# Performance work log

Hardware: AMD Instinct MI355X
Metric: run time of the kernel (lower is better)

## Reference

```python
import jax, jax.numpy as jnp
import numpy as np

SR = 16000; HOP = 160; NM = 80; FMIN = 80.0; FMAX = 8000.0
T = 4 * SR              # 64000 samples
NSTAGE = 4              # cascaded biquad stages per channel
D = 256; NH = 8; DH = 32; NL = 8; DFF = 1024
BN_EPS = 1e-5; LN_EPS = 1e-5


def _biquad_coeffs():
    fc = np.logspace(np.log10(FMIN), np.log10(FMAX), NM)           # [NM]
    q = 4.0 + 2.0 * np.arange(NSTAGE)                               # [4]
    omega = 2.0 * np.pi * fc / SR
    alpha = np.sin(omega)[None, :] / (2.0 * q[:, None])             # [4,NM]
    a0 = 1.0 + alpha
    b0 = alpha / a0
    b2 = -alpha / a0
    a1 = (-2.0 * np.cos(omega))[None, :] / a0
    a2 = (1.0 - alpha) / a0
    return tuple(jnp.asarray(c, jnp.float32) for c in (b0, b2, a1, a2))


def _cochlear(x):
    # x: [B,T] -> [B,NM,T]; 4-stage cascaded bandpass biquads, zero initial state.
    b0, b2, a1, a2 = _biquad_coeffs()
    B = x.shape[0]
    z = jnp.zeros((NSTAGE, NM, B), x.dtype)

    def body(carry, xt):
        x1, x2, y1, y2 = carry                      # each [4,NM,B]
        sig = jnp.broadcast_to(xt[None, :], (NM, B))
        nx1, nx2, ny1, ny2 = [], [], [], []
        for s in range(NSTAGE):                     # fixed small cascade
            y = (b0[s][:, None] * sig + b2[s][:, None] * x2[s]
                 - a1[s][:, None] * y1[s] - a2[s][:, None] * y2[s])
            nx1.append(sig); nx2.append(x1[s]); ny1.append(y); ny2.append(y1[s])
            sig = y
        return (jnp.stack(nx1), jnp.stack(nx2), jnp.stack(ny1), jnp.stack(ny2)), sig

    _, ys = jax.lax.scan(body, (z, z, z, z), x.T)   # ys: [T,NM,B]
    return ys.transpose(2, 1, 0)


def _ln(x, g, b):
    m = x.mean(-1, keepdims=True)
    v = jnp.mean((x - m) ** 2, -1, keepdims=True)
    return (x - m) * jax.lax.rsqrt(v + LN_EPS) * g + b


def _cbr(h, w, b, g, bb):
    h = jax.lax.conv_general_dilated(h, w, (1, 1), 'SAME',
                                     dimension_numbers=('NCHW', 'OIHW', 'NCHW'))
    h = h + b[None, :, None, None]
    # eval-mode BatchNorm2d: running_mean=0, running_var=1
    h = h * (g / np.sqrt(1.0 + BN_EPS))[None, :, None, None] + bb[None, :, None, None]
    return jax.nn.relu(h)


def _mha(x, wqkv, bqkv, wo, bo):
    B, S, _ = x.shape
    qkv = x @ wqkv.T + bqkv
    q, k, v = jnp.split(qkv, 3, axis=-1)
    heads = lambda t: t.reshape(B, S, NH, DH).transpose(0, 2, 1, 3)
    q, k, v = heads(q), heads(k), heads(v)
    attn = jax.nn.softmax(jnp.einsum('bhqd,bhkd->bhqk', q, k) / np.sqrt(DH), axis=-1)
    o = jnp.einsum('bhqk,bhkd->bhqd', attn, v).transpose(0, 2, 1, 3).reshape(B, S, D)
    return o @ wo.T + bo


def _forward(x, cw1, cb1, g1, be1, cw2, cb2, g2, be2, cw3, cb3, g3, be3,
             qkv_w, qkv_b, out_w, out_b, ln1_g, ln1_b,
             ff1_w, ff1_b, ff2_w, ff2_b, ln2_g, ln2_b, pw, pb):
    B = x.shape[0]
    sig = _cochlear(x)                                    # [B,80,T]
    env = jnp.abs(sig)
    frames = env.reshape(B, NM, T // HOP, HOP).mean(-1)   # avg_pool1d k=s=160 -> [B,80,400]
    feats = jnp.log(frames + 1e-8)[:, None]               # [B,1,80,400]
    h = _cbr(feats, cw1, cb1, g1, be1)
    h = _cbr(h, cw2, cb2, g2, be2)
    h = _cbr(h, cw3, cb3, g3, be3)                        # [B,256,80,400]
    # AdaptiveAvgPool2d((80,32)): H already 80 (identity); pool W 400->32 with torch bin rule
    W_in, W_out = h.shape[-1], 32
    bins = [(int(np.floor(i * W_in / W_out)), int(np.ceil((i + 1) * W_in / W_out)))
            for i in range(W_out)]
    h = jnp.stack([h[..., s:e].mean(-1) for s, e in bins], axis=-1)   # [B,256,80,32]
    tok = h.reshape(B, D, -1).transpose(0, 2, 1)          # [B,2560,256]
    for l in range(NL):   # post-norm encoder layer, relu FFN, dropout=0 (eval)
        a = _mha(tok, qkv_w[l], qkv_b[l], out_w[l], out_b[l])
        tok = _ln(tok + a, ln1_g[l], ln1_b[l])
        f = jax.nn.relu(tok @ ff1_w[l].T + ff1_b[l]) @ ff2_w[l].T + ff2_b[l]
        tok = _ln(tok + f, ln2_g[l], ln2_b[l])
    return tok @ pw.T + pb                                # [B,2560,512]


def setup_inputs() -> dict:
    key = jax.random.key(0)
    ks = jax.random.split(key, 16)
    w = lambda k, shape, std=0.02: jax.random.normal(k, shape, jnp.float32) * std
    return {
        'x': jax.random.normal(ks[0], (1, T), jnp.float32),
        'cw1': w(ks[1], (64, 1, 3, 3), 0.1), 'cb1': jnp.zeros((64,)),
        'g1': jnp.ones((64,)), 'be1': jnp.zeros((64,)),
        'cw2': w(ks[2], (128, 64, 3, 3), 0.05), 'cb2': jnp.zeros((128,)),
        'g2': jnp.ones((128,)), 'be2': jnp.zeros((128,)),
        'cw3': w(ks[3], (256, 128, 3, 3), 0.05), 'cb3': jnp.zeros((256,)),
        'g3': jnp.ones((256,)), 'be3': jnp.zeros((256,)),
        'qkv_w': w(ks[4], (NL, 3 * D, D)), 'qkv_b': jnp.zeros((NL, 3 * D)),
        'out_w': w(ks[5], (NL, D, D)), 'out_b': jnp.zeros((NL, D)),
        'ln1_g': jnp.ones((NL, D)), 'ln1_b': jnp.zeros((NL, D)),
        'ff1_w': w(ks[6], (NL, DFF, D)), 'ff1_b': jnp.zeros((NL, DFF)),
        'ff2_w': w(ks[7], (NL, D, DFF)), 'ff2_b': jnp.zeros((NL, D)),
        'ln2_g': jnp.ones((NL, D)), 'ln2_b': jnp.zeros((NL, D)),
        'pw': w(ks[8], (512, D)), 'pb': jnp.zeros((512,)),
    }


def reference(x, cw1, cb1, g1, be1, cw2, cb2, g2, be2, cw3, cb3, g3, be3,
              qkv_w, qkv_b, out_w, out_b, ln1_g, ln1_b,
              ff1_w, ff1_b, ff2_w, ff2_b, ln2_g, ln2_b, pw, pb):
    return _forward(x, cw1, cb1, g1, be1, cw2, cb2, g2, be2, cw3, cb3, g3, be3,
                    qkv_w, qkv_b, out_w, out_b, ln1_g, ln1_b,
                    ff1_w, ff1_b, ff2_w, ff2_b, ln2_g, ln2_b, pw, pb)
```

## Files before the change

kernel.cpp:

```cpp
#include <hip/hip_runtime.h>
#include <hip/hip_bf16.h>
#include <math.h>

typedef __hip_bfloat16 bf16;
typedef short s16x8 __attribute__((ext_vector_type(8)));
typedef float f32x4 __attribute__((ext_vector_type(4)));

__device__ __forceinline__ float b2f(const bf16 v) { return __bfloat162float(v); }
__device__ __forceinline__ float ldf(int isbf, const void* p, size_t i) {
    return isbf ? __bfloat162float(((const bf16*)p)[i]) : ((const float*)p)[i];
}
__device__ __forceinline__ double ldd(int isbf, const void* p, size_t i) {
    return (double)ldf(isbf, p, i);
}
__device__ __forceinline__ short sbf(float f) {
    bf16 h = __float2bfloat16(f);
    return *(short*)&h;
}
__device__ __forceinline__ s16x8 cvt8(float4 a, float4 b) {
    union { bf16 h[8]; s16x8 v; } u;
    u.h[0] = __float2bfloat16(a.x); u.h[1] = __float2bfloat16(a.y);
    u.h[2] = __float2bfloat16(a.z); u.h[3] = __float2bfloat16(a.w);
    u.h[4] = __float2bfloat16(b.x); u.h[5] = __float2bfloat16(b.y);
    u.h[6] = __float2bfloat16(b.z); u.h[7] = __float2bfloat16(b.w);
    return u.v;
}

#define TLEN   64000
#define NMEL   80
#define CHUNK  160
#define NCHK   400
#define SEQ    2560
#define DMODEL 256
#define PI_D   3.14159265358979323846
#define CLW    420

#define F_COEF  0ul
#define F_FLAG  2560ul
#define F_M     2576ul
#define F_V     12816ul
#define F_INI   524816ul
#define F_FEATS 1036816ul
#define F_TOK   1068816ul
#define F_BIG   1724176ul
#define O_C1CL  0ul
#define O_C2CL  1102080ul
#define O_C3    3306240ul
#define O_WTB2  11500000ul
#define O_WTB3  11540000ul

__global__ void k_detect(const unsigned short* __restrict__ g, int* __restrict__ flag) {
    if (threadIdx.x == 0 && blockIdx.x == 0) *flag = (g[0] == 0x3F80) ? 1 : 0;
}

__global__ void k_coeffs(double* __restrict__ cf) {
    int i = blockIdx.x * 256 + threadIdx.x;
    if (i >= 4 * NMEL) return;
    int s = i / NMEL, m = i % NMEL;
    double lg0 = log10(80.0), lg1 = log10(8000.0);
    double fc = pow(10.0, lg0 + (lg1 - lg0) * (double)m / 79.0);
    double q = 4.0 + 2.0 * (double)s;
    double omega = 2.0 * PI_D * fc / 16000.0;
    double al = sin(omega) / (2.0 * q);
    double a0 = 1.0 + al;
    cf[i * 4 + 0] = (double)(float)(al / a0);
    cf[i * 4 + 1] = (double)(float)(-al / a0);
    cf[i * 4 + 2] = (double)(float)(-2.0 * cos(omega) / a0);
    cf[i * 4 + 3] = (double)(float)((1.0 - al) / a0);
}

__global__ __launch_bounds__(256) void k_bqf_zero(const void* __restrict__ x,
        const double* __restrict__ cf, const int* __restrict__ flagp,
        double* __restrict__ v) {
    int i = blockIdx.x * 256 + threadIdx.x;
    if (i >= NMEL * NCHK) return;
    int isbf = *flagp;
    int j = i / NMEL, m = i % NMEL;
    double b0[4], b2[4], a1[4], a2[4];
#pragma unroll
    for (int s = 0; s < 4; ++s) {
        const double* c = &cf[(s * NMEL + m) * 4];
        b0[s] = c[0]; b2[s] = c[1]; a1[s] = c[2]; a2[s] = c[3];
    }
    int t0 = j * CHUNK;
    double x1 = (t0 > 0) ? ldd(isbf, x, t0 - 1) : 0.0;
    double x2 = (t0 > 1) ? ldd(isbf, x, t0 - 2) : 0.0;
    double s0 = 0, s1 = 0, s2 = 0, s3 = 0, s4 = 0, s5 = 0, s6 = 0, s7 = 0;
    for (int t = t0; t < t0 + CHUNK; ++t) {
        double xt = ldd(isbf, x, t);
        double y0 = fma(b0[0], xt, fma(b2[0], x2, fma(-a1[0], s0, -a2[0] * s1)));
        double y1 = fma(b0[1], y0, fma(b2[1], s1, fma(-a1[1], s2, -a2[1] * s3)));
        double y2 = fma(b0[2], y1, fma(b2[2], s3, fma(-a1[2], s4, -a2[2] * s5)));
        double y3 = fma(b0[3], y2, fma(b2[3], s5, fma(-a1[3], s6, -a2[3] * s7)));
        s1 = s0; s0 = y0; s3 = s2; s2 = y1; s5 = s4; s4 = y2; s7 = s6; s6 = y3;
        x2 = x1; x1 = xt;
    }
    double* vp = &v[((size_t)m * NCHK + j) * 8];
    vp[0] = s0; vp[1] = s1; vp[2] = s2; vp[3] = s3;
    vp[4] = s4; vp[5] = s5; vp[6] = s6; vp[7] = s7;
}

__global__ __launch_bounds__(256) void k_bqA(const double* __restrict__ cf,
                                             double* __restrict__ M) {
    __shared__ double P[4][8][8], R[4][8][8], T[4][8][8];
    int t = threadIdx.x;
    int cg = t >> 6, e8 = t & 63;
    int i = e8 >> 3, jj = e8 & 7;
    int m = blockIdx.x * 4 + cg;
    double b0[4], b2[4], a1[4], a2[4];
#pragma unroll
    for (int s = 0; s < 4; ++s) {
        const double* c = &cf[(s * NMEL + m) * 4];
        b0[s] = c[0]; b2[s] = c[1]; a1[s] = c[2]; a2[s] = c[3];
    }
    double s[8];
#pragma unroll
    for (int k = 0; k < 8; ++k) s[k] = (k == jj) ? 1.0 : 0.0;
    double y0 = fma(-a1[0], s[0], -a2[0] * s[1]);
    double y1 = fma(b0[1], y0, fma(b2[1], s[1], fma(-a1[1], s[2], -a2[1] * s[3])));
    double y2 = fma(b0[2], y1, fma(b2[2], s[3], fma(-a1[2], s[4], -a2[2] * s[5])));
    double y3 = fma(b0[3], y2, fma(b2[3], s[5], fma(-a1[3], s[6], -a2[3] * s[7])));
    double colv[8] = {y0, s[0], y1, s[2], y2, s[4], y3, s[6]};
    P[cg][i][jj] = colv[i];
    R[cg][i][jj] = (i == jj) ? 1.0 : 0.0;
    __syncthreads();
    int e = CHUNK;
    while (e) {
        double acc = 0.0;
#pragma unroll
        for (int k = 0; k < 8; ++k) acc = fma(R[cg][i][k], P[cg][k][jj], acc);
        T[cg][i][jj] = acc;
        __syncthreads();
        if (e & 1) R[cg][i][jj] = T[cg][i][jj];
        __syncthreads();
        acc = 0.0;
#pragma unroll
        for (int k = 0; k < 8; ++k) acc = fma(P[cg][i][k], P[cg][k][jj], acc);
        T[cg][i][jj] = acc;
        __syncthreads();
        P[cg][i][jj] = T[cg][i][jj];
        e >>= 1;
        __syncthreads();
    }
    M[(size_t)m * 64 + i * 8 + jj] = R[cg][i][jj];
}

__global__ __launch_bounds__(512) void k_bq_scan8p(const double* __restrict__ Mbuf,
        const double* __restrict__ v, double* __restrict__ ini) {
    __shared__ double Mp[9][64];
    __shared__ double bufA[NCHK][8];
    __shared__ double bufB[NCHK][8];
    int m = blockIdx.x, t = threadIdx.x;
    if (t < 64) Mp[0][t] = Mbuf[(size_t)m * 64 + t];
    __syncthreads();
    for (int s = 1; s < 9; ++s) {
        if (t < 64) {
            int i = t >> 3, jj = t & 7;
            double acc = 0.0;
#pragma unroll
            for (int k = 0; k < 8; ++k) acc = fma(Mp[s - 1][i * 8 + k], Mp[s - 1][k * 8 + jj], acc);
            Mp[s][t] = acc;
        }
        __syncthreads();
    }
    double b[8];
    if (t < NCHK) {
        const double* vp = &v[((size_t)m * NCHK + t) * 8];
#pragma unroll
        for (int i = 0; i < 8; ++i) { b[i] = vp[i]; bufA[t][i] = b[i]; }
    }
    __syncthreads();
#pragma unroll
    for (int s = 0; s < 9; ++s) {
        int off = 1 << s;
        double nb[8];
        if (t < NCHK) {
            if (t >= off) {
                const double* src = (s & 1) ? bufB[t - off] : bufA[t - off];
#pragma unroll
                for (int i = 0; i < 8; ++i) {
                    double acc = b[i];
#pragma unroll
                    for (int k = 0; k < 8; ++k) acc = fma(Mp[s][i * 8 + k], src[k], acc);
                    nb[i] = acc;
                }
            } else {
#pragma unroll
                for (int i = 0; i < 8; ++i) nb[i] = b[i];
            }
        }
        __syncthreads();
        if (t < NCHK) {
            double* dst = (s & 1) ? bufA[t] : bufB[t];
#pragma unroll
            for (int i = 0; i < 8; ++i) { dst[i] = nb[i]; b[i] = nb[i]; }
        }
        __syncthreads();
    }
    if (t < NCHK) {
        double* op = &ini[((size_t)m * NCHK + t) * 8];
        if (t == 0) {
#pragma unroll
            for (int i = 0; i < 8; ++i) op[i] = 0.0;
        } else {
#pragma unroll
            for (int i = 0; i < 8; ++i) op[i] = bufB[t - 1][i];
        }
    }
}

__global__ __launch_bounds__(256) void k_bqf_emit(const void* __restrict__ x,
        const double* __restrict__ cf, const int* __restrict__ flagp,
        const double* __restrict__ ini, float* __restrict__ feats) {
    int i = blockIdx.x * 256 + threadIdx.x;
    if (i >= NMEL * NCHK) return;
    int isbf = *flagp;
    int j = i / NMEL, m = i % NMEL;
    double b0[4], b2[4], a1[4], a2[4];
#pragma unroll
    for (int s = 0; s < 4; ++s) {
        const double* c = &cf[(s * NMEL + m) * 4];
        b0[s] = c[0]; b2[s] = c[1]; a1[s] = c[2]; a2[s] = c[3];
    }
    int t0 = j * CHUNK;
    double x1 = (t0 > 0) ? ldd(isbf, x, t0 - 1) : 0.0;
    double x2 = (t0 > 1) ? ldd(isbf, x, t0 - 2) : 0.0;
    const double* ip = &ini[((size_t)m * NCHK + j) * 8];
    double s0 = ip[0], s1 = ip[1], s2 = ip[2], s3 = ip[3];
    double s4 = ip[4], s5 = ip[5], s6 = ip[6], s7 = ip[7];
    double acc = 0.0;
    for (int t = t0; t < t0 + CHUNK; ++t) {
        double xt = ldd(isbf, x, t);
        double y0 = fma(b0[0], xt, fma(b2[0], x2, fma(-a1[0], s0, -a2[0] * s1)));
        double y1 = fma(b0[1], y0, fma(b2[1], s1, fma(-a1[1], s2, -a2[1] * s3)));
        double y2 = fma(b0[2], y1, fma(b2[2], s3, fma(-a1[2], s4, -a2[2] * s5)));
        double y3 = fma(b0[3], y2, fma(b2[3], s5, fma(-a1[3], s6, -a2[3] * s7)));
        acc += fabs(y3);
        s1 = s0; s0 = y0; s3 = s2; s2 = y1; s5 = s4; s4 = y2; s7 = s6; s6 = y3;
        x2 = x1; x1 = xt;
    }
    feats[(size_t)m * 400 + j] = (float)log(acc * (1.0 / 160.0) + 1e-8);
}

__global__ void k_fill0(bf16* __restrict__ p, int n8) {
    int i = blockIdx.x * 256 + threadIdx.x;
    if (i < n8) { s16x8 z = {}; ((s16x8*)p)[i] = z; }
}

__global__ void k_wtb(const void* __restrict__ w, const int* __restrict__ flagp,
                      bf16* __restrict__ out, int CO, int CIN) {
    int i = blockIdx.x * 256 + threadIdx.x;
    int K = CIN * 9;
    if (i >= CO * K) return;
    int co = i / K, rem = i % K;
    int c = rem / 288, tp = (rem / 32) % 9, cin = rem & 31;
    out[i] = __float2bfloat16(ldf(*flagp, w, ((size_t)co * CIN + c * 32 + cin) * 9 + tp));
}

__global__ __launch_bounds__(256) void k_conv1cl(const float* __restrict__ in,
        const void* __restrict__ wt, const void* __restrict__ bi,
        const void* __restrict__ ga, const void* __restrict__ be,
        const int* __restrict__ flagp, bf16* __restrict__ out) {
    __shared__ float wsh[576];
    __shared__ float ash[64];
    __shared__ float bsh[64];
    int t = threadIdx.x;
    int isbf = *flagp;
    for (int i = t; i < 576; i += 256) wsh[i] = ldf(isbf, wt, i);
    if (t < 64) {
        float A = ldf(isbf, ga, t) * 0.999995000037f;
        ash[t] = A;
        bsh[t] = fmaf(ldf(isbf, bi, t), A, ldf(isbf, be, t));
    }
    __syncthreads();
    int i = blockIdx.x * 256 + t;
    if (i >= 32000) return;
    int h = i / 400, w = i % 400;
    float xs[9];
#pragma unroll
    for (int dy = 0; dy < 3; ++dy)
#pragma unroll
        for (int dx = 0; dx < 3; ++dx) {
            int hh = h + dy - 1, ww = w + dx - 1;
            xs[dy * 3 + dx] = (hh >= 0 && hh < 80 && ww >= 0 && ww < 400)
                              ? in[hh * 400 + ww] : 0.f;
        }
    bf16* op = out + ((size_t)(h + 1) * CLW + (w + 1)) * 64;
#pragma unroll
    for (int g = 0; g < 8; ++g) {
        union { bf16 h8[8]; s16x8 v; } u;
#pragma unroll
        for (int e = 0; e < 8; ++e) {
            int co = g * 8 + e;
            float acc = 0.f;
#pragma unroll
            for (int uu = 0; uu < 9; ++uu) acc = fmaf(wsh[co * 9 + uu], xs[uu], acc);
            u.h8[e] = __float2bfloat16(fmaxf(fmaf(acc, ash[co], bsh[co]), 0.f));
        }
        *(s16x8*)&op[g * 8] = u.v;
    }
}

template<int CIN, int CO, int CLOUT>
__global__ __launch_bounds__(256) void k_convm(const bf16* __restrict__ cl,
        const bf16* __restrict__ Wtb,
        const void* __restrict__ bi, const void* __restrict__ ga,
        const void* __restrict__ be, const int* __restrict__ flagp,
        void* __restrict__ out) {
    const int MT = CO / 64;
    const int K = CIN * 9;
    __shared__ short Bs[4][36][40];
    int t = threadIdx.x, wv = t >> 6, L = t & 63, quad = L >> 4, lx = L & 15;
    int w0 = blockIdx.x * 32, h0 = blockIdx.y * 2;
    int cob = wv * (CO / 4);
    f32x4 acc[MT][2][2] = {};
    for (int c = 0; c < CIN / 32; ++c) {
        __syncthreads();
        for (int u = t; u < 544; u += 256) {
            int seg = u >> 2, part = u & 3;
            int dy = seg / 34, ww = seg % 34;
            *(s16x8*)&Bs[dy][ww][part * 8] =
                *(const s16x8*)&cl[((size_t)(h0 + dy) * CLW + (w0 + ww)) * CIN + c * 32 + part * 8];
        }
        __syncthreads();
#pragma unroll
        for (int tp = 0; tp < 9; ++tp) {
            int dy = tp / 3, dx = tp % 3;
            int kbase = (c * 9 + tp) * 32;
            s16x8 af[MT];
#pragma unroll
            for (int mt = 0; mt < MT; ++mt)
                af[mt] = *(const s16x8*)&Wtb[(size_t)(cob + mt * 16 + lx) * K + kbase + quad * 8];
#pragma unroll
            for (int hr = 0; hr < 2; ++hr) {
#pragma unroll
                for (int n = 0; n < 2; ++n) {
                    s16x8 bfr = *(const s16x8*)&Bs[dy + hr][n * 16 + lx + dx][quad * 8];
#pragma unroll
                    for (int mt = 0; mt < MT; ++mt)
                        acc[mt][hr][n] = __builtin_amdgcn_mfma_f32_16x16x32_bf16(af[mt], bfr, acc[mt][hr][n], 0, 0, 0);
                }
            }
        }
    }
    int isbf = *flagp;
#pragma unroll
    for (int mt = 0; mt < MT; ++mt) {
#pragma unroll
        for (int r = 0; r < 4; ++r) {
            int co = cob + mt * 16 + quad * 4 + r;
            float A = ldf(isbf, ga, co) * 0.999995000037f;
            float B = fmaf(ldf(isbf, bi, co), A, ldf(isbf, be, co));
#pragma unroll
            for (int hr = 0; hr < 2; ++hr) {
                int h = h0 + hr;
#pragma unroll
                for (int n = 0; n < 2; ++n) {
                    int w = w0 + n * 16 + lx;
                    if (w < 400) {
                        float v = fmaxf(fmaf(acc[mt][hr][n][r], A, B), 0.f);
                        if (CLOUT)
                            ((bf16*)out)[((size_t)(h + 1) * CLW + (w + 1)) * CO + co] = __float2bfloat16(v);
                        else
                            ((float*)out)[(size_t)co * 32000 + h * 400 + w] = v;
                    }
                }
            }
        }
    }
}

__global__ __launch_bounds__(256) void k_pool(const float* __restrict__ c3,
                                              float* __restrict__ tok) {
    int i = blockIdx.x * 256 + threadIdx.x;
    if (i >= SEQ * DMODEL) return;
    int s = i >> 8, c = i & 255;
    int f = s >> 5, jj = s & 31;
    int w0 = (jj * 25) >> 1;
    const float* p = c3 + ((size_t)c * 80 + f) * 400 + w0;
    float sum = 0.f;
#pragma unroll
    for (int k = 0; k < 13; ++k) sum += p[k];
    tok[i] = sum * (1.f / 13.f);
}

template<int RELU, int OUTMODE, int NT, int ACOMB, int ABF16>
__global__ __launch_bounds__(256) void k_gemm(const void* __restrict__ A,
        const void* __restrict__ W, size_t woff,
        const void* __restrict__ bias, size_t boff,
        const int* __restrict__ flagp, void* __restrict__ Cout_,
        bf16* __restrict__ vtb, const float* __restrict__ partb,
        int M, int N, int K) {
    __shared__ short As[64][136];
    __shared__ short Bs[NT * 16][136];
    const int isbf = *flagp;
    int t = threadIdx.x;
    int wv = t >> 6, L = t & 63, quad = L >> 4, lx = L & 15;
    int row0 = blockIdx.y * 64, col0 = blockIdx.x * (NT * 16);
    f32x4 acc[NT] = {};
    for (int k0 = 0; k0 < K; k0 += 128) {
        __syncthreads();
        {
            int row = t >> 2, cb = (t & 3) * 8;
#pragma unroll
            for (int c = 0; c < 4; ++c) {
                int col = cb + c * 32;
                s16x8 av;
                if (ACOMB) {
                    int q = row0 + row;
                    int kk = k0 + col;
                    int hh = kk >> 5, d = kk & 31;
                    const float* pa = partb + ((size_t)(hh * 2) * SEQ + q) * 36;
                    const float* pc = pa + (size_t)SEQ * 36;
                    float m0 = pa[32], l0 = pa[33], m1 = pc[32], l1 = pc[33];
                    float Mx = fmaxf(m0, m1);
                    float e0 = __expf(m0 - Mx), e1 = __expf(m1 - Mx);
                    float inv = 1.f / (l0 * e0 + l1 * e1);
                    float4 u0 = *(const float4*)(pa + d), u1 = *(const float4*)(pa + d + 4);
                    float4 v0 = *(const float4*)(pc + d), v1 = *(const float4*)(pc + d + 4);
                    float4 r0, r1;
                    r0.x = (u0.x * e0 + v0.x * e1) * inv; r0.y = (u0.y * e0 + v0.y * e1) * inv;
                    r0.z = (u0.z * e0 + v0.z * e1) * inv; r0.w = (u0.w * e0 + v0.w * e1) * inv;
                    r1.x = (u1.x * e0 + v1.x * e1) * inv; r1.y = (u1.y * e0 + v1.y * e1) * inv;
                    r1.z = (u1.z * e0 + v1.z * e1) * inv; r1.w = (u1.w * e0 + v1.w * e1) * inv;
                    av = cvt8(r0, r1);
                } else if (ABF16) {
                    av = *(const s16x8*)((const bf16*)A + (size_t)(row0 + row) * K + k0 + col);
                } else {
                    const float* ap = (const float*)A + (size_t)(row0 + row) * K + k0 + col;
                    av = cvt8(*(const float4*)ap, *(const float4*)(ap + 4));
                }
                *(s16x8*)&As[row][col] = av;
            }
        }
        if (NT == 4) {
            int row = t >> 2, cb = (t & 3) * 8;
#pragma unroll
            for (int c = 0; c < 4; ++c) {
                int col = cb + c * 32;
                size_t widx = woff + (size_t)(col0 + row) * K + k0 + col;
                s16x8 wv8;
                if (isbf) {
                    wv8 = *(const s16x8*)((const bf16*)W + widx);
                } else {
                    const float* wf = (const float*)W + widx;
                    wv8 = cvt8(*(const float4*)wf, *(const float4*)(wf + 4));
                }
                *(s16x8*)&Bs[row][col] = wv8;
            }
        } else {
            int row = t >> 3, cb = (t & 7) * 8;
#pragma unroll
            for (int c = 0; c < 2; ++c) {
                int col = cb + c * 64;
                size_t widx = woff + (size_t)(col0 + row) * K + k0 + col;
                s16x8 wv8;
                if (isbf) {
                    wv8 = *(const s16x8*)((const bf16*)W + widx);
                } else {
                    const float* wf = (const float*)W + widx;
                    wv8 = cvt8(*(const float4*)wf, *(const float4*)(wf + 4));
                }
                *(s16x8*)&Bs[row][col] = wv8;
            }
        }
        __syncthreads();
#pragma unroll
        for (int kc = 0; kc < 4; ++kc) {
            s16x8 af = *(const s16x8*)&As[wv * 16 + lx][kc * 32 + quad * 8];
#pragma unroll
            for (int n = 0; n < NT; ++n) {
                s16x8 bf_ = *(const s16x8*)&Bs[n * 16 + lx][kc * 32 + quad * 8];
                acc[n] = __builtin_amdgcn_mfma_f32_16x16x32_bf16(af, bf_, acc[n], 0, 0, 0);
            }
        }
    }
#pragma unroll
    for (int n = 0; n < NT; ++n) {
        int col = col0 + n * 16 + lx;
        float bv = ldf(isbf, bias, boff + col);
#pragma unroll
        for (int r = 0; r < 4; ++r) {
            int row = row0 + wv * 16 + quad * 4 + r;
            float val = acc[n][r] + bv;
            if (RELU) val = fmaxf(val, 0.f);
            if (OUTMODE == 0) {
                ((float*)Cout_)[(size_t)row * N + col] = val;
            } else if (OUTMODE == 2) {
                bf16 bb_ = __float2bfloat16(val);
                ((bf16*)Cout_)[(size_t)row * N + col] = bb_;
                if (col >= 512) vtb[(size_t)(col - 512) * SEQ + row] = bb_;
            } else if (OUTMODE == 3) {
                ((bf16*)Cout_)[(size_t)row * N + col] = __float2bfloat16(val);
            } else {
                if (isbf) ((bf16*)Cout_)[(size_t)row * N + col] = __float2bfloat16(val);
                else      ((float*)Cout_)[(size_t)row * N + col] = val;
            }
        }
    }
}

__global__ __launch_bounds__(256) void k_flash(const bf16* __restrict__ qkvB,
        const bf16* __restrict__ vtb, float* __restrict__ part) {
    int b = blockIdx.x;
    int pp = b & 1, qb = (b >> 1) % 40, h = b / 80;
    int t = threadIdx.x, wv = t >> 6, L = t & 63, quad = L >> 4, lx = L & 15;
    int q0 = qb * 64;
    __shared__ short Qs[64][40];
    __shared__ short Ks[64][40];
    __shared__ short Vt[32][72];
    __shared__ short Ps[64][72];
    const float scale = 0.17677669529663687f;
    int sr = t >> 2, sk = (t & 3) * 8;
    *(s16x8*)&Qs[sr][sk] = *(const s16x8*)&qkvB[(size_t)(q0 + sr) * 768 + h * 32 + sk];
    f32x4 o[2] = {};
    float mrow[4], lrow[4];
#pragma unroll
    for (int r = 0; r < 4; ++r) { mrow[r] = -INFINITY; lrow[r] = 0.f; }
    int kstart = pp * 1280;
    int vd = t >> 3, vk = (t & 7) * 8;
    for (int kt = 0; kt < 20; ++kt) {
        int kb = kstart + kt * 64;
        __syncthreads();
        *(s16x8*)&Ks[sr][sk] = *(const s16x8*)&qkvB[(size_t)(kb + sr) * 768 + 256 + h * 32 + sk];
        *(s16x8*)&Vt[vd][vk] = *(const s16x8*)&vtb[(size_t)(h * 32 + vd) * SEQ + kb + vk];
        __syncthreads();
        s16x8 qf = *(const s16x8*)&Qs[wv * 16 + lx][quad * 8];
        f32x4 sc[4] = {};
#pragma unroll
        for (int n = 0; n < 4; ++n) {
            s16x8 kf = *(const s16x8*)&Ks[n * 16 + lx][quad * 8];
            sc[n] = __builtin_amdgcn_mfma_f32_16x16x32_bf16(qf, kf, sc[n], 0, 0, 0);
        }
#pragma unroll
        for (int r = 0; r < 4; ++r) {
            float tm = -INFINITY;
#pragma unroll
            for (int n = 0; n < 4; ++n) { sc[n][r] *= scale; tm = fmaxf(tm, sc[n][r]); }
#pragma unroll
            for (int mk = 1; mk < 16; mk <<= 1) tm = fmaxf(tm, __shfl_xor(tm, mk));
            float mn = fmaxf(mrow[r], tm);
            float al = __expf(mrow[r] - mn);
            float ps = 0.f;
#pragma unroll
            for (int n = 0; n < 4; ++n) {
                float e = __expf(sc[n][r] - mn);
                sc[n][r] = e; ps += e;
            }
#pragma unroll
            for (int mk = 1; mk < 16; mk <<= 1) ps += __shfl_xor(ps, mk);
            lrow[r] = lrow[r] * al + ps;
            mrow[r] = mn;
            o[0][r] *= al; o[1][r] *= al;
            int qrow = wv * 16 + quad * 4 + r;
#pragma unroll
            for (int n = 0; n < 4; ++n) Ps[qrow][n * 16 + lx] = sbf(sc[n][r]);
        }
        __syncthreads();
#pragma unroll
        for (int ks = 0; ks < 2; ++ks) {
            s16x8 pf = *(const s16x8*)&Ps[wv * 16 + lx][ks * 32 + quad * 8];
#pragma unroll
            for (int n = 0; n < 2; ++n) {
                s16x8 vf = *(const s16x8*)&Vt[n * 16 + lx][ks * 32 + quad * 8];
                o[n] = __builtin_amdgcn_mfma_f32_16x16x32_bf16(pf, vf, o[n], 0, 0, 0);
            }
        }
    }
#pragma unroll
    for (int r = 0; r < 4; ++r) {
        int q = q0 + wv * 16 + quad * 4 + r;
        size_t pb_ = ((size_t)(h * 2 + pp) * SEQ + q) * 36;
        part[pb_ + lx] = o[0][r];
        part[pb_ + 16 + lx] = o[1][r];
        if (lx == 0) { part[pb_ + 32] = mrow[r]; part[pb_ + 33] = lrow[r]; }
    }
}

__global__ __launch_bounds__(256) void k_ln(float* __restrict__ tok,
        const float* __restrict__ res, const void* __restrict__ gg,
        const void* __restrict__ bb, size_t goff, const int* __restrict__ flagp) {
    int isbf = *flagp;
    int row = blockIdx.x * 4 + (threadIdx.x >> 6);
    int lane = threadIdx.x & 63;
    float* tp = tok + (size_t)row * DMODEL;
    const float* rp = res + (size_t)row * DMODEL;
    float4 a = *(const float4*)&tp[lane * 4];
    float4 r = *(const float4*)&rp[lane * 4];
    float x0 = a.x + r.x, x1 = a.y + r.y, x2 = a.z + r.z, x3 = a.w + r.w;
    float s = x0 + x1 + x2 + x3;
#pragma unroll
    for (int mk = 1; mk < 64; mk <<= 1) s += __shfl_xor(s, mk);
    float mean = s * (1.f / 256.f);
    float d0 = x0 - mean, d1 = x1 - mean, d2 = x2 - mean, d3 = x3 - mean;
    float vs = d0 * d0 + d1 * d1 + d2 * d2 + d3 * d3;
#pragma unroll
    for (int mk = 1; mk < 64; mk <<= 1) vs += __shfl_xor(vs, mk);
    float rstd = rsqrtf(vs * (1.f / 256.f) + 1e-5f);
    size_t c = goff + lane * 4;
    float y0 = fmaf(d0 * rstd, ldf(isbf, gg, c + 0), ldf(isbf, bb, c + 0));
    float y1 = fmaf(d1 * rstd, ldf(isbf, gg, c + 1), ldf(isbf, bb, c + 1));
    float y2 = fmaf(d2 * rstd, ldf(isbf, gg, c + 2), ldf(isbf, bb, c + 2));
    float y3 = fmaf(d3 * rstd, ldf(isbf, gg, c + 3), ldf(isbf, bb, c + 3));
    *(float4*)&tp[lane * 4] = make_float4(y0, y1, y2, y3);
}

extern "C" void kernel_launch(void* const* d_in, const int* in_sizes, int n_in,
                              void* d_out, int out_size, void* d_ws, size_t ws_size,
                              hipStream_t stream) {
    const void* x    = d_in[0];
    const void* cw1  = d_in[1];  const void* cb1 = d_in[2];
    const void* g1   = d_in[3];  const void* be1 = d_in[4];
    const void* cw2  = d_in[5];  const void* cb2 = d_in[6];
    const void* g2   = d_in[7];  const void* be2 = d_in[8];
    const void* cw3  = d_in[9];  const void* cb3 = d_in[10];
    const void* g3   = d_in[11]; const void* be3 = d_in[12];
    const void* qkvw = d_in[13]; const void* qkvb = d_in[14];
    const void* outw = d_in[15]; const void* outb = d_in[16];
    const void* ln1g = d_in[17]; const void* ln1b = d_in[18];
    const void* ff1w = d_in[19]; const void* ff1b = d_in[20];
    const void* ff2w = d_in[21]; const void* ff2b = d_in[22];
    const void* ln2g = d_in[23]; const void* ln2b = d_in[24];
    const void* pw   = d_in[25]; const void* pb   = d_in[26];

    float*  ws    = (float*)d_ws;
    double* coef  = (double*)(ws + F_COEF);
    int*    flagp = (int*)(ws + F_FLAG);
    double* Mbuf  = (double*)(ws + F_M);
    double* vbuf  = (double*)(ws + F_V);
    double* ini   = (double*)(ws + F_INI);
    float*  feats = ws + F_FEATS;
    float*  tok   = ws + F_TOK;
    bf16*   c1cl  = (bf16*)(ws + F_BIG + O_C1CL);
    bf16*   c2cl  = (bf16*)(ws + F_BIG + O_C2CL);
    float*  c3    = ws + F_BIG + O_C3;
    bf16*   Wtb2  = (bf16*)(ws + F_BIG + O_WTB2);
    bf16*   Wtb3  = (bf16*)(ws + F_BIG + O_WTB3);
    bf16*   qkvB  = (bf16*)(ws + F_BIG);
    bf16*   vtb   = (bf16*)(ws + F_BIG + 983040ul);
    float*  partb = ws + F_BIG + 1310720ul;
    float*  proj  = ws + F_BIG + 2785280ul;
    bf16*   ff1bf = (bf16*)(ws + F_BIG + 3440640ul);

    k_detect<<<dim3(1), dim3(64), 0, stream>>>((const unsigned short*)ln1g, flagp);
    k_coeffs<<<dim3(2), dim3(256), 0, stream>>>(coef);
    k_wtb<<<dim3(288), dim3(256), 0, stream>>>(cw2, flagp, Wtb2, 128, 64);
    k_wtb<<<dim3(1152), dim3(256), 0, stream>>>(cw3, flagp, Wtb3, 256, 128);

    k_bqA<<<dim3(20), dim3(256), 0, stream>>>(coef, Mbuf);
    k_bqf_zero<<<dim3(125), dim3(256), 0, stream>>>(x, coef, flagp, vbuf);
    k_bq_scan8p<<<dim3(80), dim3(512), 0, stream>>>(Mbuf, vbuf, ini);
    k_bqf_emit<<<dim3(125), dim3(256), 0, stream>>>(x, coef, flagp, ini, feats);

    k_fill0<<<dim3(1077), dim3(256), 0, stream>>>(c1cl, 275520);
    k_fill0<<<dim3(2153), dim3(256), 0, stream>>>(c2cl, 551040);
    k_conv1cl<<<dim3(125), dim3(256), 0, stream>>>(feats, cw1, cb1, g1, be1, flagp, c1cl);
    k_convm<64, 128, 1><<<dim3(13, 40), dim3(256), 0, stream>>>(
        c1cl, Wtb2, cb2, g2, be2, flagp, c2cl);
    k_convm<128, 256, 0><<<dim3(13, 40), dim3(256), 0, stream>>>(
        c2cl, Wtb3, cb3, g3, be3, flagp, c3);

    k_pool<<<dim3(2560), dim3(256), 0, stream>>>(c3, tok);

    for (int l = 0; l < 8; ++l) {
        k_gemm<0, 2, 4, 0, 0><<<dim3(12, 40), dim3(256), 0, stream>>>(
            tok, qkvw, (size_t)l * 768 * 256, qkvb, (size_t)l * 768,
            flagp, qkvB, vtb, nullptr, SEQ, 768, 256);
        k_flash<<<dim3(640), dim3(256), 0, stream>>>(qkvB, vtb, partb);
        k_gemm<0, 0, 2, 1, 0><<<dim3(8, 40), dim3(256), 0, stream>>>(
            nullptr, outw, (size_t)l * 256 * 256, outb, (size_t)l * 256,
            flagp, proj, nullptr, partb, SEQ, 256, 256);
        k_ln<<<dim3(640), dim3(256), 0, stream>>>(tok, proj, ln1g, ln1b, (size_t)l * 256, flagp);
        k_gemm<1, 3, 4, 0, 0><<<dim3(16, 40), dim3(256), 0, stream>>>(
            tok, ff1w, (size_t)l * 1024 * 256, ff1b, (size_t)l * 1024,
            flagp, ff1bf, nullptr, nullptr, SEQ, 1024, 256);
        k_gemm<0, 0, 2, 0, 1><<<dim3(8, 40), dim3(256), 0, stream>>>(
            ff1bf, ff2w, (size_t)l * 256 * 1024, ff2b, (size_t)l * 256,
            flagp, proj, nullptr, nullptr, SEQ, 256, 1024);
        k_ln<<<dim3(640), dim3(256), 0, stream>>>(tok, proj, ln2g, ln2b, (size_t)l * 256, flagp);
    }

    k_gemm<0, 1, 2, 0, 0><<<dim3(16, 40), dim3(256), 0, stream>>>(
        tok, pw, 0ul, pb, 0ul, flagp, d_out, nullptr, nullptr, SEQ, 512, 256);
}
```

Measured before the change: 1.194 ms.

## Split conv channels across grid z, split flash keys 4-way, shrink GEMM K tile

Convolution output channels are split across two blocks in grid z, halving per-block MMA work and doubling block count. Flash attention now splits the key range into four partitions instead of two, doubling the number of blocks, and the combine step in the out-projection GEMM merges four partial softmax results. The GEMM K tile is halved to 64, which reduces shared memory per block and may raise occupancy, at the cost of more loop iterations and barriers. Workspace offsets are moved to fit the larger partial buffer.

```diff
diff --git a/kernel.cpp b/kernel.cpp
--- a/kernel.cpp
+++ b/kernel.cpp
@@ -307,12 +307,12 @@
         const void* __restrict__ bi, const void* __restrict__ ga,
         const void* __restrict__ be, const int* __restrict__ flagp,
         void* __restrict__ out) {
-    const int MT = CO / 64;
+    const int MT = CO / 128;
     const int K = CIN * 9;
     __shared__ short Bs[4][36][40];
     int t = threadIdx.x, wv = t >> 6, L = t & 63, quad = L >> 4, lx = L & 15;
     int w0 = blockIdx.x * 32, h0 = blockIdx.y * 2;
-    int cob = wv * (CO / 4);
+    int cob = blockIdx.z * (CO / 2) + wv * (CO / 8);
     f32x4 acc[MT][2][2] = {};
     for (int c = 0; c < CIN / 32; ++c) {
         __syncthreads();
@@ -391,39 +391,42 @@
         const int* __restrict__ flagp, void* __restrict__ Cout_,
         bf16* __restrict__ vtb, const float* __restrict__ partb,
         int M, int N, int K) {
-    __shared__ short As[64][136];
-    __shared__ short Bs[NT * 16][136];
+    __shared__ short As[64][72];
+    __shared__ short Bs[NT * 16][72];
     const int isbf = *flagp;
     int t = threadIdx.x;
     int wv = t >> 6, L = t & 63, quad = L >> 4, lx = L & 15;
     int row0 = blockIdx.y * 64, col0 = blockIdx.x * (NT * 16);
     f32x4 acc[NT] = {};
-    for (int k0 = 0; k0 < K; k0 += 128) {
+    for (int k0 = 0; k0 < K; k0 += 64) {
         __syncthreads();
         {
             int row = t >> 2, cb = (t & 3) * 8;
 #pragma unroll
-            for (int c = 0; c < 4; ++c) {
+            for (int c = 0; c < 2; ++c) {
                 int col = cb + c * 32;
                 s16x8 av;
                 if (ACOMB) {
                     int q = row0 + row;
                     int kk = k0 + col;
                     int hh = kk >> 5, d = kk & 31;
-                    const float* pa = partb + ((size_t)(hh * 2) * SEQ + q) * 36;
-                    const float* pc = pa + (size_t)SEQ * 36;
-                    float m0 = pa[32], l0 = pa[33], m1 = pc[32], l1 = pc[33];
-                    float Mx = fmaxf(m0, m1);
+                    const float* p0 = partb + ((size_t)(hh * 4) * SEQ + q) * 36;
+                    const size_t ps = (size_t)SEQ * 36;
+                    float m0 = p0[32], m1 = p0[ps + 32], m2 = p0[2 * ps + 32], m3 = p0[3 * ps + 32];
+                    float Mx = fmaxf(fmaxf(m0, m1), fmaxf(m2, m3));
                     float e0 = __expf(m0 - Mx), e1 = __expf(m1 - Mx);
-                    float inv = 1.f / (l0 * e0 + l1 * e1);
-                    float4 u0 = *(const float4*)(pa + d), u1 = *(const float4*)(pa + d + 4);
-                    float4 v0 = *(const float4*)(pc + d), v1 = *(const float4*)(pc + d + 4);
-                    float4 r0, r1;
-                    r0.x = (u0.x * e0 + v0.x * e1) * inv; r0.y = (u0.y * e0 + v0.y * e1) * inv;
-                    r0.z = (u0.z * e0 + v0.z * e1) * inv; r0.w = (u0.w * e0 + v0.w * e1) * inv;
-                    r1.x = (u1.x * e0 + v1.x * e1) * inv; r1.y = (u1.y * e0 + v1.y * e1) * inv;
-                    r1.z = (u1.z * e0 + v1.z * e1) * inv; r1.w = (u1.w * e0 + v1.w * e1) * inv;
-                    av = cvt8(r0, r1);
+                    float e2 = __expf(m2 - Mx), e3 = __expf(m3 - Mx);
+                    float inv = 1.f / (p0[33] * e0 + p0[ps + 33] * e1 +
+                                       p0[2 * ps + 33] * e2 + p0[3 * ps + 33] * e3);
+                    float rr[8];
+#pragma unroll
+                    for (int u = 0; u < 8; ++u) {
+                        float num = p0[d + u] * e0 + p0[ps + d + u] * e1 +
+                                    p0[2 * ps + d + u] * e2 + p0[3 * ps + d + u] * e3;
+                        rr[u] = num * inv;
+                    }
+                    av = cvt8(make_float4(rr[0], rr[1], rr[2], rr[3]),
+                              make_float4(rr[4], rr[5], rr[6], rr[7]));
                 } else if (ABF16) {
                     av = *(const s16x8*)((const bf16*)A + (size_t)(row0 + row) * K + k0 + col);
                 } else {
@@ -436,7 +439,7 @@
         if (NT == 4) {
             int row = t >> 2, cb = (t & 3) * 8;
 #pragma unroll
-            for (int c = 0; c < 4; ++c) {
+            for (int c = 0; c < 2; ++c) {
                 int col = cb + c * 32;
                 size_t widx = woff + (size_t)(col0 + row) * K + k0 + col;
                 s16x8 wv8;
@@ -449,24 +452,20 @@
                 *(s16x8*)&Bs[row][col] = wv8;
             }
         } else {
-            int row = t >> 3, cb = (t & 7) * 8;
-#pragma unroll
-            for (int c = 0; c < 2; ++c) {
-                int col = cb + c * 64;
-                size_t widx = woff + (size_t)(col0 + row) * K + k0 + col;
-                s16x8 wv8;
-                if (isbf) {
-                    wv8 = *(const s16x8*)((const bf16*)W + widx);
-                } else {
-                    const float* wf = (const float*)W + widx;
-                    wv8 = cvt8(*(const float4*)wf, *(const float4*)(wf + 4));
-                }
-                *(s16x8*)&Bs[row][col] = wv8;
-            }
-        }
-        __syncthreads();
-#pragma unroll
-        for (int kc = 0; kc < 4; ++kc) {
+            int row = t >> 3, col = (t & 7) * 8;
+            size_t widx = woff + (size_t)(col0 + row) * K + k0 + col;
+            s16x8 wv8;
+            if (isbf) {
+                wv8 = *(const s16x8*)((const bf16*)W + widx);
+            } else {
+                const float* wf = (const float*)W + widx;
+                wv8 = cvt8(*(const float4*)wf, *(const float4*)(wf + 4));
+            }
+            *(s16x8*)&Bs[row][col] = wv8;
+        }
+        __syncthreads();
+#pragma unroll
+        for (int kc = 0; kc < 2; ++kc) {
             s16x8 af = *(const s16x8*)&As[wv * 16 + lx][kc * 32 + quad * 8];
 #pragma unroll
             for (int n = 0; n < NT; ++n) {
@@ -503,7 +502,7 @@
 __global__ __launch_bounds__(256) void k_flash(const bf16* __restrict__ qkvB,
         const bf16* __restrict__ vtb, float* __restrict__ part) {
     int b = blockIdx.x;
-    int pp = b & 1, qb = (b >> 1) % 40, h = b / 80;
+    int pp = b & 3, qb = (b >> 2) % 40, h = b / 160;
     int t = threadIdx.x, wv = t >> 6, L = t & 63, quad = L >> 4, lx = L & 15;
     int q0 = qb * 64;
     __shared__ short Qs[64][40];
@@ -517,9 +516,9 @@
     float mrow[4], lrow[4];
 #pragma unroll
     for (int r = 0; r < 4; ++r) { mrow[r] = -INFINITY; lrow[r] = 0.f; }
-    int kstart = pp * 1280;
+    int kstart = pp * 640;
     int vd = t >> 3, vk = (t & 7) * 8;
-    for (int kt = 0; kt < 20; ++kt) {
+    for (int kt = 0; kt < 10; ++kt) {
         int kb = kstart + kt * 64;
         __syncthreads();
         *(s16x8*)&Ks[sr][sk] = *(const s16x8*)&qkvB[(size_t)(kb + sr) * 768 + 256 + h * 32 + sk];
@@ -570,7 +569,7 @@
 #pragma unroll
     for (int r = 0; r < 4; ++r) {
         int q = q0 + wv * 16 + quad * 4 + r;
-        size_t pb_ = ((size_t)(h * 2 + pp) * SEQ + q) * 36;
+        size_t pb_ = ((size_t)(h * 4 + pp) * SEQ + q) * 36;
         part[pb_ + lx] = o[0][r];
         part[pb_ + 16 + lx] = o[1][r];
         if (lx == 0) { part[pb_ + 32] = mrow[r]; part[pb_ + 33] = lrow[r]; }
@@ -639,8 +638,8 @@
     bf16*   qkvB  = (bf16*)(ws + F_BIG);
     bf16*   vtb   = (bf16*)(ws + F_BIG + 983040ul);
     float*  partb = ws + F_BIG + 1310720ul;
-    float*  proj  = ws + F_BIG + 2785280ul;
-    bf16*   ff1bf = (bf16*)(ws + F_BIG + 3440640ul);
+    float*  proj  = ws + F_BIG + 4259840ul;
+    bf16*   ff1bf = (bf16*)(ws + F_BIG + 4915200ul);
 
     k_detect<<<dim3(1), dim3(64), 0, stream>>>((const unsigned short*)ln1g, flagp);
     k_coeffs<<<dim3(2), dim3(256), 0, stream>>>(coef);
@@ -655,9 +654,9 @@
     k_fill0<<<dim3(1077), dim3(256), 0, stream>>>(c1cl, 275520);
     k_fill0<<<dim3(2153), dim3(256), 0, stream>>>(c2cl, 551040);
     k_conv1cl<<<dim3(125), dim3(256), 0, stream>>>(feats, cw1, cb1, g1, be1, flagp, c1cl);
-    k_convm<64, 128, 1><<<dim3(13, 40), dim3(256), 0, stream>>>(
+    k_convm<64, 128, 1><<<dim3(13, 40, 2), dim3(256), 0, stream>>>(
         c1cl, Wtb2, cb2, g2, be2, flagp, c2cl);
-    k_convm<128, 256, 0><<<dim3(13, 40), dim3(256), 0, stream>>>(
+    k_convm<128, 256, 0><<<dim3(13, 40, 2), dim3(256), 0, stream>>>(
         c2cl, Wtb3, cb3, g3, be3, flagp, c3);
 
     k_pool<<<dim3(2560), dim3(256), 0, stream>>>(c3, tok);
@@ -666,7 +665,7 @@
         k_gemm<0, 2, 4, 0, 0><<<dim3(12, 40), dim3(256), 0, stream>>>(
             tok, qkvw, (size_t)l * 768 * 256, qkvb, (size_t)l * 768,
             flagp, qkvB, vtb, nullptr, SEQ, 768, 256);
-        k_flash<<<dim3(640), dim3(256), 0, stream>>>(qkvB, vtb, partb);
+        k_flash<<<dim3(1280), dim3(256), 0, stream>>>(qkvB, vtb, partb);
         k_gemm<0, 0, 2, 1, 0><<<dim3(8, 40), dim3(256), 0, stream>>>(
             nullptr, outw, (size_t)l * 256 * 256, outb, (size_t)l * 256,
             flagp, proj, nullptr, partb, SEQ, 256, 256);
```

After: 1.199 ms. No clear change (+0.4%).
